# Optimization experiments

Hardware: AMD Instinct MI355X
Metric: run time of the kernel (lower is better)

## Reference

```python
import jax, jax.numpy as jnp
import numpy as np

V, E_DIM, H, B, T = 390, 256, 512, 64, 512
START = 388


def setup_inputs() -> dict:
    key = jax.random.key(0)
    ks = jax.random.split(key, 32)
    s = 0.05
    rn = lambda k, shape: jax.random.normal(k, shape, jnp.float32) * s
    inp = {
        "input": jax.random.normal(ks[0], (B, T, V), jnp.float32),
        # encoder params
        "enc_emb": rn(ks[1], (V, E_DIM)),
        "enc_Wih0": rn(ks[2], (3 * H, E_DIM)),
        "enc_Whh0": rn(ks[3], (3 * H, H)),
        "enc_bih0": rn(ks[4], (3 * H,)),
        "enc_bhh0": rn(ks[5], (3 * H,)),
        "enc_Wih1": rn(ks[6], (3 * H, H)),
        "enc_Whh1": rn(ks[7], (3 * H, H)),
        "enc_bih1": rn(ks[8], (3 * H,)),
        "enc_bhh1": rn(ks[9], (3 * H,)),
        # decoder params
        "dec_emb": rn(ks[10], (V, E_DIM)),
        "dec_Wih0": rn(ks[11], (3 * H, E_DIM)),
        "dec_Whh0": rn(ks[12], (3 * H, H)),
        "dec_bih0": rn(ks[13], (3 * H,)),
        "dec_bhh0": rn(ks[14], (3 * H,)),
        "dec_Wih1": rn(ks[15], (3 * H, H)),
        "dec_Whh1": rn(ks[16], (3 * H, H)),
        "dec_bih1": rn(ks[17], (3 * H,)),
        "dec_bhh1": rn(ks[18], (3 * H,)),
        # prediction head
        "Wp1": rn(ks[19], (H, H)),
        "bp1": rn(ks[20], (H,)),
        "Wp2": rn(ks[21], (V, H)),
        "bp2": rn(ks[22], (V,)),
    }
    return inp


def _gru_cell(x, h, Wih, Whh, bih, bhh):
    # PyTorch GRU cell: gates ordered (r, z, n)
    gi = x @ Wih.T + bih
    gh = h @ Whh.T + bhh
    ir, iz, inn = jnp.split(gi, 3, axis=-1)
    hr, hz, hn = jnp.split(gh, 3, axis=-1)
    r = jax.nn.sigmoid(ir + hr)
    z = jax.nn.sigmoid(iz + hz)
    n = jnp.tanh(inn + r * hn)
    return (1.0 - z) * n + z * h


def reference(input, enc_emb, enc_Wih0, enc_Whh0, enc_bih0, enc_bhh0,
              enc_Wih1, enc_Whh1, enc_bih1, enc_bhh1,
              dec_emb, dec_Wih0, dec_Whh0, dec_bih0, dec_bhh0,
              dec_Wih1, dec_Whh1, dec_bih1, dec_bhh1,
              Wp1, bp1, Wp2, bp2):
    batch, max_len, vocab = input.shape
    hdim = enc_Whh0.shape[1]

    # ---- Encoder: soft embedding + 2-layer GRU, keep final hidden states ----
    x = jnp.einsum('btv,ve->bte', input, enc_emb)  # [B,T,E]
    xt = jnp.transpose(x, (1, 0, 2))               # time-major [T,B,E]
    h0 = jnp.zeros((batch, hdim), input.dtype)

    def step0(h, xt_):
        h = _gru_cell(xt_, h, enc_Wih0, enc_Whh0, enc_bih0, enc_bhh0)
        return h, h
    h1_enc, seq1 = jax.lax.scan(step0, h0, xt)

    def step1(h, xt_):
        h = _gru_cell(xt_, h, enc_Wih1, enc_Whh1, enc_bih1, enc_bhh1)
        return h, None
    h2_enc, _ = jax.lax.scan(step1, h0, seq1)

    tok0 = jnp.full((batch,), START, jnp.int32)
    rng0 = jax.random.key(42)

    def dec_step(carry, _):
        h1, h2, tok, rng = carry
        rng, sk = jax.random.split(rng)
        xe = dec_emb[tok]                               # [B,E]
        h1 = _gru_cell(xe, h1, dec_Wih0, dec_Whh0, dec_bih0, dec_bhh0)
        h2 = _gru_cell(h1, h2, dec_Wih1, dec_Whh1, dec_bih1, dec_bhh1)
        hid = h2 @ Wp1.T + bp1
        hid = jnp.where(hid >= 0, hid, 0.1 * hid)       # LeakyReLU(0.1)
        logits = hid @ Wp2.T + bp2                      # temp=1 -> logits/temp == logits
        probs = jax.nn.softmax(logits, axis=-1)
        tok = jax.random.categorical(sk, logits, axis=-1).astype(jnp.int32)
        return (h1, h2, tok, rng), (probs, tok)

    _, (probs_seq, toks) = jax.lax.scan(
        dec_step, (h1_enc, h2_enc, tok0, rng0), None, length=max_len - 1)

    start_oh = jax.nn.one_hot(tok0, vocab, dtype=input.dtype)  # [B,V]
    outputs = jnp.concatenate(
        [start_oh[:, None, :], jnp.transpose(probs_seq, (1, 0, 2))], axis=1)
    max_output = jnp.concatenate(
        [jnp.full((batch, 1), float(START), jnp.float32),
         toks.T.astype(jnp.float32)], axis=1)
    return outputs, max_output
```

## Files before the change

kernel.cpp:

```cpp
#include <hip/hip_runtime.h>
#include <math.h>


#define BB 64
#define TT 512
#define VV 390
#define EE 256
#define HH 512

#define SW(k, b) ((((k) >> 2) << 8) + ((b) << 2) + ((k) & 3))

static __device__ __forceinline__ void tf2x32(unsigned k0, unsigned k1,
                                              unsigned x0, unsigned x1,
                                              unsigned &o0, unsigned &o1) {
  unsigned ks2 = k0 ^ k1 ^ 0x1BD11BDAu;
  x0 += k0; x1 += k1;
#define TFR(r) x0 += x1; x1 = (x1 << (r)) | (x1 >> (32 - (r))); x1 ^= x0;
  TFR(13) TFR(15) TFR(26) TFR(6)
  x0 += k1; x1 += ks2 + 1u;
  TFR(17) TFR(29) TFR(16) TFR(24)
  x0 += ks2; x1 += k0 + 2u;
  TFR(13) TFR(15) TFR(26) TFR(6)
  x0 += k0; x1 += k1 + 3u;
  TFR(17) TFR(29) TFR(16) TFR(24)
  x0 += k1; x1 += ks2 + 4u;
  TFR(13) TFR(15) TFR(26) TFR(6)
  x0 += ks2; x1 += k0 + 5u;
#undef TFR
  o0 = x0; o1 = x1;
}

static __device__ __forceinline__ float sigm(float x) {
  return 1.0f / (1.0f + expf(-x));
}

static __device__ __forceinline__ unsigned ldu_a(const unsigned* p) {
  return __hip_atomic_load((unsigned*)p, __ATOMIC_RELAXED,
                           __HIP_MEMORY_SCOPE_AGENT);
}
static __device__ __forceinline__ void stu_a(unsigned* p, unsigned v) {
  __hip_atomic_store(p, v, __ATOMIC_RELAXED, __HIP_MEMORY_SCOPE_AGENT);
}
static __device__ __forceinline__ float ldf_a(const float* p) {
  return __uint_as_float(ldu_a((const unsigned*)p));
}
static __device__ __forceinline__ void stf_a(float* p, float v) {
  stu_a((unsigned*)p, __float_as_uint(v));
}
static __device__ __forceinline__ float2 ldf2_a(const float* p) {
  unsigned long long v = __hip_atomic_load((unsigned long long*)p,
      __ATOMIC_RELAXED, __HIP_MEMORY_SCOPE_AGENT);
  return make_float2(__uint_as_float((unsigned)v),
                     __uint_as_float((unsigned)(v >> 32)));
}

static __device__ __forceinline__ void stage512(const float* X, int b0,
                                                float2* L) {
  int tid = threadIdx.x;
  float2 v[8];
#pragma unroll
  for (int r = 0; r < 8; ++r) {
    int i = tid + (r << 8);
    v[r] = ldf2_a(X + ((i >> 4) << 8) + ((b0 + ((i >> 1) & 7)) << 2) +
                  ((i & 1) << 1));
  }
#pragma unroll
  for (int r = 0; r < 8; ++r) L[tid + (r << 8)] = v[r];
}

template <int K>
static __device__ __forceinline__ void dot3_lds(const float4* Lx, int bi,
    const float* __restrict__ w0, const float* __restrict__ w1,
    const float* __restrict__ w2, float &r0, float &r1, float &r2) {
  const float4* q0 = (const float4*)w0;
  const float4* q1 = (const float4*)w1;
  const float4* q2 = (const float4*)w2;
  float s0 = 0.f, s1 = 0.f, s2 = 0.f;
#pragma unroll
  for (int k4 = 0; k4 < (K >> 2); ++k4) {
    float4 x = Lx[(k4 << 3) + bi];
    float4 u0 = q0[k4], u1 = q1[k4], u2 = q2[k4];
    s0 = fmaf(x.x, u0.x, s0); s0 = fmaf(x.y, u0.y, s0); s0 = fmaf(x.z, u0.z, s0); s0 = fmaf(x.w, u0.w, s0);
    s1 = fmaf(x.x, u1.x, s1); s1 = fmaf(x.y, u1.y, s1); s1 = fmaf(x.z, u1.z, s1); s1 = fmaf(x.w, u1.w, s1);
    s2 = fmaf(x.x, u2.x, s2); s2 = fmaf(x.y, u2.y, s2); s2 = fmaf(x.z, u2.z, s2); s2 = fmaf(x.w, u2.w, s2);
  }
  r0 = s0; r1 = s1; r2 = s2;
}

template <int K>
static __device__ __forceinline__ float dot1_lds(const float4* Lx, int bi,
    const float* __restrict__ w) {
  const float4* q = (const float4*)w;
  float s = 0.f;
#pragma unroll
  for (int k4 = 0; k4 < (K >> 2); ++k4) {
    float4 x = Lx[(k4 << 3) + bi];
    float4 u = q[k4];
    s = fmaf(x.x, u.x, s); s = fmaf(x.y, u.y, s);
    s = fmaf(x.z, u.z, s); s = fmaf(x.w, u.w, s);
  }
  return s;
}

template <int K>
static __device__ __forceinline__ void dot3s_p(const float* __restrict__ X, int b,
    const float* __restrict__ w0, const float* __restrict__ w1,
    const float* __restrict__ w2, float &r0, float &r1, float &r2) {
  const float4* q0 = (const float4*)w0;
  const float4* q1 = (const float4*)w1;
  const float4* q2 = (const float4*)w2;
  const float4* Xp = (const float4*)X;
  float s0 = 0.f, s1 = 0.f, s2 = 0.f;
#pragma unroll
  for (int k4 = 0; k4 < (K >> 2); ++k4) {
    float4 x = Xp[(k4 << 6) + b];
    float4 u0 = q0[k4], u1 = q1[k4], u2 = q2[k4];
    s0 = fmaf(x.x, u0.x, s0); s0 = fmaf(x.y, u0.y, s0); s0 = fmaf(x.z, u0.z, s0); s0 = fmaf(x.w, u0.w, s0);
    s1 = fmaf(x.x, u1.x, s1); s1 = fmaf(x.y, u1.y, s1); s1 = fmaf(x.z, u1.z, s1); s1 = fmaf(x.w, u1.w, s1);
    s2 = fmaf(x.x, u2.x, s2); s2 = fmaf(x.y, u2.y, s2); s2 = fmaf(x.z, u2.z, s2); s2 = fmaf(x.w, u2.w, s2);
  }
  r0 = s0; r1 = s1; r2 = s2;
}

template <int K>
static __device__ __forceinline__ void dot3_row(const float* __restrict__ xrow,
    const float* __restrict__ w0, const float* __restrict__ w1,
    const float* __restrict__ w2, float &r0, float &r1, float &r2) {
  const float4* xq = (const float4*)xrow;
  const float4* q0 = (const float4*)w0;
  const float4* q1 = (const float4*)w1;
  const float4* q2 = (const float4*)w2;
  float s0 = 0.f, s1 = 0.f, s2 = 0.f;
#pragma unroll
  for (int k4 = 0; k4 < (K >> 2); ++k4) {
    float4 x = xq[k4];
    float4 u0 = q0[k4], u1 = q1[k4], u2 = q2[k4];
    s0 = fmaf(x.x, u0.x, s0); s0 = fmaf(x.y, u0.y, s0); s0 = fmaf(x.z, u0.z, s0); s0 = fmaf(x.w, u0.w, s0);
    s1 = fmaf(x.x, u1.x, s1); s1 = fmaf(x.y, u1.y, s1); s1 = fmaf(x.z, u1.z, s1); s1 = fmaf(x.w, u1.w, s1);
    s2 = fmaf(x.x, u2.x, s2); s2 = fmaf(x.y, u2.y, s2); s2 = fmaf(x.z, u2.z, s2); s2 = fmaf(x.w, u2.w, s2);
  }
  r0 = s0; r1 = s1; r2 = s2;
}

static __device__ __forceinline__ void gbar(unsigned* f, int nwg, int wgi,
                                            unsigned ep) {
  __syncthreads();
  int tid = threadIdx.x;
  if (tid == 0) stu_a(f + wgi, ep);
  if (tid < 64) {
    bool ok;
    do {
      ok = true;
      for (int i = tid; i < nwg; i += 64) ok &= (ldu_a(f + i) >= ep);
    } while (!__all((int)ok));
  }
  __syncthreads();
}

__global__ __launch_bounds__(256) void k_init(float* out,
    float* h1buf, float* h2buf, int* tok, unsigned* ebase) {
  int wg = blockIdx.x, tid = threadIdx.x;
  for (int i = wg * 256 + tid; i < HH * BB; i += 64 * 256) {
    h1buf[i] = 0.f;
    h2buf[i] = 0.f;
  }
  for (int v = tid; v < VV; v += 256)
    out[(size_t)wg * TT * VV + v] = (v == 388) ? 1.0f : 0.0f;
  if (wg == 0) {
    ebase[tid] = 0u;
    ebase[tid + 256] = 0u;
  }
  if (tid == 0) {
    out[(size_t)BB * TT * VV + (size_t)wg * TT] = 388.0f;
    tok[wg] = 388;
  }
}

__global__ __launch_bounds__(256) void k_xgemm(const float* __restrict__ input,
    const float* __restrict__ emb, float* __restrict__ xT) {
  int t = blockIdx.x, tid = threadIdx.x;
  int s = tid >> 6, b = tid & 63;
  __shared__ float lin[64 * 65];
  float4 acc[16];
#pragma unroll
  for (int i = 0; i < 16; ++i) acc[i] = make_float4(0.f, 0.f, 0.f, 0.f);
  for (int k0 = 0; k0 < VV; k0 += 64) {
    int kmax = min(64, VV - k0);
    __syncthreads();
#pragma unroll
    for (int r = 0; r < 16; ++r) {
      int idx = r * 256 + tid;
      int b2 = idx >> 6, kk = idx & 63;
      if (kk < kmax)
        lin[kk * 65 + b2] = input[((size_t)b2 * TT + t) * VV + k0 + kk];
    }
    __syncthreads();
    for (int kk = 0; kk < kmax; ++kk) {
      float xv = lin[kk * 65 + b];
      const float4* er = (const float4*)(emb + (size_t)(k0 + kk) * EE);
#pragma unroll
      for (int i = 0; i < 16; ++i) {
        float4 w = er[s + 4 * i];
        acc[i].x = fmaf(xv, w.x, acc[i].x);
        acc[i].y = fmaf(xv, w.y, acc[i].y);
        acc[i].z = fmaf(xv, w.z, acc[i].z);
        acc[i].w = fmaf(xv, w.w, acc[i].w);
      }
    }
  }
  float* dst0 = xT + (size_t)t * (EE * 64);
#pragma unroll
  for (int i = 0; i < 16; ++i)
    *(float4*)(dst0 + (s + 4 * i) * 256 + 4 * b) = acc[i];
}

__global__ __launch_bounds__(256, 2) void k_enc(
    const float* xT, float* h1buf, float* h2buf,
    const float* __restrict__ Wih0, const float* __restrict__ Whh0,
    const float* __restrict__ bih0, const float* __restrict__ bhh0,
    const float* __restrict__ Wih1, const float* __restrict__ Whh1,
    const float* __restrict__ bih1, const float* __restrict__ bhh1,
    unsigned* eflags, unsigned* dflags) {
  int wg = blockIdx.x, tid = threadIdx.x;
  int g = wg >> 6, wgi = wg & 63;
  int b0 = g << 3;
  int lay = wgi >> 5, j0 = (wgi & 31) << 4;
  int task = tid >> 7, l = tid & 127;
  int jj = l >> 3, bi = l & 7;
  int j = j0 + jj, b = b0 + bi;
  __shared__ float2 sX[2048];
  __shared__ float2 sY[2048];
  __shared__ float part[3][128];
  unsigned* gf = eflags + (g << 6);
  for (int t = 0; t <= TT; ++t) {
    const float* h1_r = h1buf + (t & 1) * (HH * BB);
    float* h1_w = h1buf + ((t + 1) & 1) * (HH * BB);
    if (lay == 0) {
      if (t < TT) {
        stage512(h1_r, b0, sX);
        __syncthreads();
        float ar = 0.f, az = 0.f, an = 0.f;
        if (task == 0) {
          dot3s_p<EE>(xT + (size_t)t * (EE * 64), b,
                      Wih0 + (size_t)j * EE, Wih0 + (size_t)(512 + j) * EE,
                      Wih0 + (size_t)(1024 + j) * EE, ar, az, an);
        } else {
          float hr, hz, hn;
          dot3_lds<HH>((const float4*)sX, bi,
                       Whh0 + (size_t)j * HH, Whh0 + (size_t)(512 + j) * HH,
                       Whh0 + (size_t)(1024 + j) * HH, hr, hz, hn);
          part[0][l] = hr; part[1][l] = hz; part[2][l] = hn;
        }
        __syncthreads();
        if (task == 0) {
          float hr = part[0][l], hz = part[1][l], hn = part[2][l];
          float r = sigm((ar + bih0[j]) + (hr + bhh0[j]));
          float z = sigm((az + bih0[512 + j]) + (hz + bhh0[512 + j]));
          float n = tanhf((an + bih0[1024 + j]) + r * (hn + bhh0[1024 + j]));
          float hp = ((const float*)sX)[((j >> 2) << 5) + (bi << 2) + (j & 3)];
          stf_a(h1_w + SW(j, b), (1.0f - z) * n + z * hp);
        }
      }
    } else {
      if (t >= 1) {
        const float* h2_r = h2buf + ((t + 1) & 1) * (HH * BB);
        float* h2_w = h2buf + (t & 1) * (HH * BB);
        stage512(h1_r, b0, sX);
        stage512(h2_r, b0, sY);
        __syncthreads();
        float ar = 0.f, az = 0.f, an = 0.f;
        if (task == 0) {
          dot3_lds<HH>((const float4*)sX, bi,
                       Wih1 + (size_t)j * HH, Wih1 + (size_t)(512 + j) * HH,
                       Wih1 + (size_t)(1024 + j) * HH, ar, az, an);
        } else {
          float hr, hz, hn;
          dot3_lds<HH>((const float4*)sY, bi,
                       Whh1 + (size_t)j * HH, Whh1 + (size_t)(512 + j) * HH,
                       Whh1 + (size_t)(1024 + j) * HH, hr, hz, hn);
          part[0][l] = hr; part[1][l] = hz; part[2][l] = hn;
        }
        __syncthreads();
        if (task == 0) {
          float hr = part[0][l], hz = part[1][l], hn = part[2][l];
          float r = sigm((ar + bih1[j]) + (hr + bhh1[j]));
          float z = sigm((az + bih1[512 + j]) + (hz + bhh1[512 + j]));
          float n = tanhf((an + bih1[1024 + j]) + r * (hn + bhh1[1024 + j]));
          float hp = ((const float*)sY)[((j >> 2) << 5) + (bi << 2) + (j & 3)];
          stf_a(h2_w + SW(j, b), (1.0f - z) * n + z * hp);
        }
      }
    }
    if (t == 2 && wgi == 0 && tid < 32) stu_a(dflags + (g << 5) + tid, 0u);
    if (t < TT) gbar(gf, 64, wgi, (unsigned)(t + 1));
  }
}

__global__ __launch_bounds__(256, 1) void k_dec(
    float* h1buf, float* h2buf,
    const float* __restrict__ demb,
    const float* __restrict__ dWih0, const float* __restrict__ dWhh0,
    const float* __restrict__ dbih0, const float* __restrict__ dbhh0,
    const float* __restrict__ dWih1, const float* __restrict__ dWhh1,
    const float* __restrict__ dbih1, const float* __restrict__ dbhh1,
    const float* __restrict__ Wp1, const float* __restrict__ bp1,
    const float* __restrict__ Wp2, const float* __restrict__ bp2,
    float* out, int* tok, unsigned* dflags, float* hid) {
  int wg = blockIdx.x, tid = threadIdx.x;
  int g = wg >> 5, wgi = wg & 31;
  int b0 = g << 3, j0 = wgi << 4;
  int task = tid >> 7, l = tid & 127;
  int jj = l >> 3, bi = l & 7;
  int j = j0 + jj, b = b0 + bi;
  __shared__ float2 sX[2048];
  __shared__ float2 sY[2048];
  __shared__ float part[3][128];
  __shared__ __align__(16) float lhid[HH];
  __shared__ float rf[8];
  __shared__ int ri[4];
  unsigned* gf = dflags + (g << 5);
  unsigned rk0 = 0u, rk1 = 42u;
  unsigned ep = 0u;
  for (int d = 0; d < TT - 1; ++d) {
    const float* h1_r = h1buf + (d & 1) * (HH * BB);
    float* h1_w = h1buf + ((d + 1) & 1) * (HH * BB);
    const float* h2_r = h2buf + (d & 1) * (HH * BB);
    float* h2_w = h2buf + ((d + 1) & 1) * (HH * BB);
    {
      stage512(h1_r, b0, sX);
      __syncthreads();
      float ar = 0.f, az = 0.f, an = 0.f;
      if (task == 1) {
        float hr, hz, hn;
        dot3_lds<HH>((const float4*)sX, bi,
                     dWhh0 + (size_t)j * HH, dWhh0 + (size_t)(512 + j) * HH,
                     dWhh0 + (size_t)(1024 + j) * HH, hr, hz, hn);
        part[0][l] = hr; part[1][l] = hz; part[2][l] = hn;
      } else {
        int tk = (int)ldu_a((const unsigned*)tok + b);
        dot3_row<EE>(demb + (size_t)tk * EE,
                     dWih0 + (size_t)j * EE, dWih0 + (size_t)(512 + j) * EE,
                     dWih0 + (size_t)(1024 + j) * EE, ar, az, an);
      }
      __syncthreads();
      if (task == 0) {
        float hr = part[0][l], hz = part[1][l], hn = part[2][l];
        float r = sigm((ar + dbih0[j]) + (hr + dbhh0[j]));
        float z = sigm((az + dbih0[512 + j]) + (hz + dbhh0[512 + j]));
        float n = tanhf((an + dbih0[1024 + j]) + r * (hn + dbhh0[1024 + j]));
        float hp = ((const float*)sX)[((j >> 2) << 5) + (bi << 2) + (j & 3)];
        stf_a(h1_w + SW(j, b), (1.0f - z) * n + z * hp);
      }
    }
    gbar(gf, 32, wgi, ++ep);
    {
      stage512(h1_w, b0, sX);
      stage512(h2_r, b0, sY);
      __syncthreads();
      float ar = 0.f, az = 0.f, an = 0.f;
      if (task == 0) {
        dot3_lds<HH>((const float4*)sX, bi,
                     dWih1 + (size_t)j * HH, dWih1 + (size_t)(512 + j) * HH,
                     dWih1 + (size_t)(1024 + j) * HH, ar, az, an);
      } else {
        float hr, hz, hn;
        dot3_lds<HH>((const float4*)sY, bi,
                     dWhh1 + (size_t)j * HH, dWhh1 + (size_t)(512 + j) * HH,
                     dWhh1 + (size_t)(1024 + j) * HH, hr, hz, hn);
        part[0][l] = hr; part[1][l] = hz; part[2][l] = hn;
      }
      __syncthreads();
      if (task == 0) {
        float hr = part[0][l], hz = part[1][l], hn = part[2][l];
        float r = sigm((ar + dbih1[j]) + (hr + dbhh1[j]));
        float z = sigm((az + dbih1[512 + j]) + (hz + dbhh1[512 + j]));
        float n = tanhf((an + dbih1[1024 + j]) + r * (hn + dbhh1[1024 + j]));
        float hp = ((const float*)sY)[((j >> 2) << 5) + (bi << 2) + (j & 3)];
        stf_a(h2_w + SW(j, b), (1.0f - z) * n + z * hp);
      }
    }
    gbar(gf, 32, wgi, ++ep);
    {
      stage512(h2_w, b0, sX);
      __syncthreads();
      if (tid < 128) {
        float a = dot1_lds<HH>((const float4*)sX, bi, Wp1 + (size_t)j * HH);
        a += bp1[j];
        stf_a(hid + SW(j, b), (a >= 0.f) ? a : 0.1f * a);
      }
    }
    gbar(gf, 32, wgi, ++ep);
    if (wgi < 8) {
      int brow = b0 + wgi;
      if (tid < 128) {
        float2 ha = ldf2_a(hid + tid * 256 + brow * 4);
        float2 hb = ldf2_a(hid + tid * 256 + brow * 4 + 2);
        lhid[4 * tid] = ha.x; lhid[4 * tid + 1] = ha.y;
        lhid[4 * tid + 2] = hb.x; lhid[4 * tid + 3] = hb.y;
      }
      __syncthreads();
      float v0 = 0.f, v1 = 0.f;
      if (tid < VV) {
        const float4* w = (const float4*)(Wp2 + (size_t)tid * HH);
        float a = 0.f;
#pragma unroll 8
        for (int k4 = 0; k4 < HH / 4; ++k4) {
          float4 q = w[k4];
          float4 hv = *(const float4*)&lhid[k4 * 4];
          a = fmaf(hv.x, q.x, a); a = fmaf(hv.y, q.y, a);
          a = fmaf(hv.z, q.z, a); a = fmaf(hv.w, q.w, a);
        }
        v0 = a + bp2[tid];
      }
      if (tid + 256 < VV) {
        const float4* w = (const float4*)(Wp2 + (size_t)(tid + 256) * HH);
        float a = 0.f;
#pragma unroll 8
        for (int k4 = 0; k4 < HH / 4; ++k4) {
          float4 q = w[k4];
          float4 hv = *(const float4*)&lhid[k4 * 4];
          a = fmaf(hv.x, q.x, a); a = fmaf(hv.y, q.y, a);
          a = fmaf(hv.z, q.z, a); a = fmaf(hv.w, q.w, a);
        }
        v1 = a + bp2[tid + 256];
      }
      float m = -INFINITY;
      if (tid < VV) m = fmaxf(m, v0);
      if (tid + 256 < VV) m = fmaxf(m, v1);
      for (int off = 32; off > 0; off >>= 1) m = fmaxf(m, __shfl_down(m, off, 64));
      if ((tid & 63) == 0) rf[tid >> 6] = m;
      __syncthreads();
      if (tid == 0) rf[4] = fmaxf(fmaxf(rf[0], rf[1]), fmaxf(rf[2], rf[3]));
      __syncthreads();
      m = rf[4];
      unsigned sk0, sk1;
      tf2x32(rk0, rk1, 0u, 1u, sk0, sk1);
      float by = -INFINITY; int bc = 0x7fffffff;
      if (tid < VV) {
        unsigned o0, o1;
        tf2x32(sk0, sk1, 0u, (unsigned)(brow * VV + tid), o0, o1);
        unsigned bits = o0 ^ o1;
        float f = __uint_as_float(0x3f800000u | (bits >> 9)) - 1.0f;
        float u = (f > 0.f) ? f : 1.17549435e-38f;
        float gg = (float)(-log(-log((double)u)));
        float y = v0 + gg;
        if (y > by || (y == by && tid < bc)) { by = y; bc = tid; }
      }
      if (tid + 256 < VV) {
        int c = tid + 256;
        unsigned o0, o1;
        tf2x32(sk0, sk1, 0u, (unsigned)(brow * VV + c), o0, o1);
        unsigned bits = o0 ^ o1;
        float f = __uint_as_float(0x3f800000u | (bits >> 9)) - 1.0f;
        float u = (f > 0.f) ? f : 1.17549435e-38f;
        float gg = (float)(-log(-log((double)u)));
        float y = v1 + gg;
        if (y > by || (y == by && c < bc)) { by = y; bc = c; }
      }
      for (int off = 32; off > 0; off >>= 1) {
        float oy = __shfl_down(by, off, 64);
        int oc = __shfl_down(bc, off, 64);
        if (oy > by || (oy == by && oc < bc)) { by = oy; bc = oc; }
      }
      if ((tid & 63) == 0) { rf[tid >> 6] = by; ri[tid >> 6] = bc; }
      __syncthreads();
      if (tid == 0) {
        by = rf[0]; bc = ri[0];
        for (int w2 = 1; w2 < 4; ++w2)
          if (rf[w2] > by || (rf[w2] == by && ri[w2] < bc)) { by = rf[w2]; bc = ri[w2]; }
        stu_a((unsigned*)tok + brow, (unsigned)bc);
        out[(size_t)BB * TT * VV + (size_t)brow * TT + (d + 1)] = (float)bc;
      }
      __syncthreads();
      float e0 = 0.f, e1 = 0.f, ssum = 0.f;
      if (tid < VV) { e0 = expf(v0 - m); ssum += e0; }
      if (tid + 256 < VV) { e1 = expf(v1 - m); ssum += e1; }
      for (int off = 32; off > 0; off >>= 1) ssum += __shfl_down(ssum, off, 64);
      if ((tid & 63) == 0) rf[tid >> 6] = ssum;
      __syncthreads();
      if (tid == 0) rf[4] = (rf[0] + rf[1]) + (rf[2] + rf[3]);
      __syncthreads();
      float S = rf[4];
      float* orow = out + ((size_t)brow * TT + (d + 1)) * VV;
      if (tid < VV) orow[tid] = e0 / S;
      if (tid + 256 < VV) orow[tid + 256] = e1 / S;
    }
    {
      unsigned n0, n1;
      tf2x32(rk0, rk1, 0u, 0u, n0, n1);
      rk0 = n0; rk1 = n1;
    }
    if (d < TT - 2) gbar(gf, 32, wgi, ++ep);
  }
}

extern "C" void kernel_launch(void* const* d_in, const int* in_sizes, int n_in,
                              void* d_out, int out_size, void* d_ws, size_t ws_size,
                              hipStream_t stream) {
  (void)in_sizes; (void)n_in; (void)out_size; (void)ws_size;
  const float* input = (const float*)d_in[0];
  const float* e_emb = (const float*)d_in[1];
  const float* eWih0 = (const float*)d_in[2];
  const float* eWhh0 = (const float*)d_in[3];
  const float* ebih0 = (const float*)d_in[4];
  const float* ebhh0 = (const float*)d_in[5];
  const float* eWih1 = (const float*)d_in[6];
  const float* eWhh1 = (const float*)d_in[7];
  const float* ebih1 = (const float*)d_in[8];
  const float* ebhh1 = (const float*)d_in[9];
  const float* d_emb = (const float*)d_in[10];
  const float* dWih0 = (const float*)d_in[11];
  const float* dWhh0 = (const float*)d_in[12];
  const float* dbih0 = (const float*)d_in[13];
  const float* dbhh0 = (const float*)d_in[14];
  const float* dWih1 = (const float*)d_in[15];
  const float* dWhh1 = (const float*)d_in[16];
  const float* dbih1 = (const float*)d_in[17];
  const float* dbhh1 = (const float*)d_in[18];
  const float* Wp1   = (const float*)d_in[19];
  const float* bp1   = (const float*)d_in[20];
  const float* Wp2   = (const float*)d_in[21];
  const float* bp2   = (const float*)d_in[22];
  float* out = (float*)d_out;

  float* xT = (float*)d_ws;
  float* h1buf = xT + (size_t)TT * EE * 64;
  float* h2buf = h1buf + 2 * HH * BB;
  int* tok = (int*)(h2buf + 2 * HH * BB);
  unsigned* eflags = (unsigned*)(out + ((size_t)1 * TT + 1) * VV);
  unsigned* dflags = (unsigned*)xT;
  float* hid = xT + 4096;

  k_init<<<64, 256, 0, stream>>>(out, h1buf, h2buf, tok, eflags);
  k_xgemm<<<TT, 256, 0, stream>>>(input, e_emb, xT);
  k_enc<<<512, 256, 0, stream>>>(xT, h1buf, h2buf,
      eWih0, eWhh0, ebih0, ebhh0, eWih1, eWhh1, ebih1, ebhh1, eflags, dflags);
  k_dec<<<256, 256, 0, stream>>>(h1buf, h2buf, d_emb,
      dWih0, dWhh0, dbih0, dbhh0, dWih1, dWhh1, dbih1, dbhh1,
      Wp1, bp1, Wp2, bp2, out, tok, dflags, hid);
}
```

Before: 73.42 ms.

## Restructure decoder step to precompute recurrent matvecs and drop a grid barrier

The decoder loop now computes the Whh0/Whh1 recurrent matvecs for the next step at the end of the current step, so each step's critical path carries only the input-side GEMV. The Wp1 projection is computed redundantly inside the head workgroups, which removes the global hid buffer and one grid barrier per step. Staging loads are rotated per workgroup to spread memory contention, and the barrier spin adds s_sleep. In exchange the head workgroups take on extra Wp1 work, and both task halves now run full 512-wide dot products.

```diff
diff --git a/kernel.cpp b/kernel.cpp
--- a/kernel.cpp
+++ b/kernel.cpp
@@ -41,9 +41,6 @@
 static __device__ __forceinline__ void stu_a(unsigned* p, unsigned v) {
   __hip_atomic_store(p, v, __ATOMIC_RELAXED, __HIP_MEMORY_SCOPE_AGENT);
 }
-static __device__ __forceinline__ float ldf_a(const float* p) {
-  return __uint_as_float(ldu_a((const unsigned*)p));
-}
 static __device__ __forceinline__ void stf_a(float* p, float v) {
   stu_a((unsigned*)p, __float_as_uint(v));
 }
@@ -55,17 +52,20 @@
 }
 
 static __device__ __forceinline__ void stage512(const float* X, int b0,
-                                                float2* L) {
+                                                float2* L, int rot) {
   int tid = threadIdx.x;
   float2 v[8];
 #pragma unroll
   for (int r = 0; r < 8; ++r) {
-    int i = tid + (r << 8);
-    v[r] = ldf2_a(X + ((i >> 4) << 8) + ((b0 + ((i >> 1) & 7)) << 2) +
-                  ((i & 1) << 1));
-  }
-#pragma unroll
-  for (int r = 0; r < 8; ++r) L[tid + (r << 8)] = v[r];
+    int idx = tid + (((r + rot) & 7) << 8);
+    v[r] = ldf2_a(X + ((idx >> 4) << 8) + ((b0 + ((idx >> 1) & 7)) << 2) +
+                  ((idx & 1) << 1));
+  }
+#pragma unroll
+  for (int r = 0; r < 8; ++r) {
+    int idx = tid + (((r + rot) & 7) << 8);
+    L[idx] = v[r];
+  }
 }
 
 template <int K>
@@ -148,11 +148,13 @@
   int tid = threadIdx.x;
   if (tid == 0) stu_a(f + wgi, ep);
   if (tid < 64) {
-    bool ok;
-    do {
-      ok = true;
+    bool done = false;
+    while (!done) {
+      bool ok = true;
       for (int i = tid; i < nwg; i += 64) ok &= (ldu_a(f + i) >= ep);
-    } while (!__all((int)ok));
+      done = __all((int)ok);
+      if (!done) __builtin_amdgcn_s_sleep(1);
+    }
   }
   __syncthreads();
 }
@@ -228,6 +230,7 @@
   int task = tid >> 7, l = tid & 127;
   int jj = l >> 3, bi = l & 7;
   int j = j0 + jj, b = b0 + bi;
+  int rot = wg & 7;
   __shared__ float2 sX[2048];
   __shared__ float2 sY[2048];
   __shared__ float part[3][128];
@@ -237,7 +240,7 @@
     float* h1_w = h1buf + ((t + 1) & 1) * (HH * BB);
     if (lay == 0) {
       if (t < TT) {
-        stage512(h1_r, b0, sX);
+        stage512(h1_r, b0, sX, rot);
         __syncthreads();
         float ar = 0.f, az = 0.f, an = 0.f;
         if (task == 0) {
@@ -265,8 +268,8 @@
       if (t >= 1) {
         const float* h2_r = h2buf + ((t + 1) & 1) * (HH * BB);
         float* h2_w = h2buf + (t & 1) * (HH * BB);
-        stage512(h1_r, b0, sX);
-        stage512(h2_r, b0, sY);
+        stage512(h1_r, b0, sX, rot);
+        stage512(h2_r, b0, sY, rot);
         __syncthreads();
         float ar = 0.f, az = 0.f, an = 0.f;
         if (task == 0) {
@@ -305,98 +308,88 @@
     const float* __restrict__ dbih1, const float* __restrict__ dbhh1,
     const float* __restrict__ Wp1, const float* __restrict__ bp1,
     const float* __restrict__ Wp2, const float* __restrict__ bp2,
-    float* out, int* tok, unsigned* dflags, float* hid) {
+    float* out, int* tok, unsigned* dflags) {
   int wg = blockIdx.x, tid = threadIdx.x;
   int g = wg >> 5, wgi = wg & 31;
   int b0 = g << 3, j0 = wgi << 4;
   int task = tid >> 7, l = tid & 127;
   int jj = l >> 3, bi = l & 7;
   int j = j0 + jj, b = b0 + bi;
+  int rot = wgi & 7;
   __shared__ float2 sX[2048];
   __shared__ float2 sY[2048];
-  __shared__ float part[3][128];
+  __shared__ float pA[3][128];
+  __shared__ float pB[3][128];
   __shared__ __align__(16) float lhid[HH];
   __shared__ float rf[8];
   __shared__ int ri[4];
+  __shared__ int ltok[8];
   unsigned* gf = dflags + (g << 5);
   unsigned rk0 = 0u, rk1 = 42u;
   unsigned ep = 0u;
+  stage512(h1buf, b0, sX, rot);
+  stage512(h2buf, b0, sY, rot);
+  __syncthreads();
+  if (task == 1) {
+    float hr, hz, hn;
+    dot3_lds<HH>((const float4*)sX, bi,
+                 dWhh0 + (size_t)j * HH, dWhh0 + (size_t)(512 + j) * HH,
+                 dWhh0 + (size_t)(1024 + j) * HH, hr, hz, hn);
+    pA[0][l] = hr; pA[1][l] = hz; pA[2][l] = hn;
+  } else {
+    float hr, hz, hn;
+    dot3_lds<HH>((const float4*)sY, bi,
+                 dWhh1 + (size_t)j * HH, dWhh1 + (size_t)(512 + j) * HH,
+                 dWhh1 + (size_t)(1024 + j) * HH, hr, hz, hn);
+    pB[0][l] = hr; pB[1][l] = hz; pB[2][l] = hn;
+  }
+  __syncthreads();
   for (int d = 0; d < TT - 1; ++d) {
-    const float* h1_r = h1buf + (d & 1) * (HH * BB);
     float* h1_w = h1buf + ((d + 1) & 1) * (HH * BB);
-    const float* h2_r = h2buf + (d & 1) * (HH * BB);
     float* h2_w = h2buf + ((d + 1) & 1) * (HH * BB);
-    {
-      stage512(h1_r, b0, sX);
-      __syncthreads();
-      float ar = 0.f, az = 0.f, an = 0.f;
-      if (task == 1) {
-        float hr, hz, hn;
-        dot3_lds<HH>((const float4*)sX, bi,
-                     dWhh0 + (size_t)j * HH, dWhh0 + (size_t)(512 + j) * HH,
-                     dWhh0 + (size_t)(1024 + j) * HH, hr, hz, hn);
-        part[0][l] = hr; part[1][l] = hz; part[2][l] = hn;
-      } else {
-        int tk = (int)ldu_a((const unsigned*)tok + b);
-        dot3_row<EE>(demb + (size_t)tk * EE,
-                     dWih0 + (size_t)j * EE, dWih0 + (size_t)(512 + j) * EE,
-                     dWih0 + (size_t)(1024 + j) * EE, ar, az, an);
-      }
-      __syncthreads();
-      if (task == 0) {
-        float hr = part[0][l], hz = part[1][l], hn = part[2][l];
-        float r = sigm((ar + dbih0[j]) + (hr + dbhh0[j]));
-        float z = sigm((az + dbih0[512 + j]) + (hz + dbhh0[512 + j]));
-        float n = tanhf((an + dbih0[1024 + j]) + r * (hn + dbhh0[1024 + j]));
-        float hp = ((const float*)sX)[((j >> 2) << 5) + (bi << 2) + (j & 3)];
-        stf_a(h1_w + SW(j, b), (1.0f - z) * n + z * hp);
-      }
+    if (tid < 8) ltok[tid] = (int)ldu_a((const unsigned*)tok + b0 + tid);
+    __syncthreads();
+    if (task == 0) {
+      int tk = ltok[bi];
+      float ar, az, an;
+      dot3_row<EE>(demb + (size_t)tk * EE,
+                   dWih0 + (size_t)j * EE, dWih0 + (size_t)(512 + j) * EE,
+                   dWih0 + (size_t)(1024 + j) * EE, ar, az, an);
+      float hr = pA[0][l], hz = pA[1][l], hn = pA[2][l];
+      float r = sigm((ar + dbih0[j]) + (hr + dbhh0[j]));
+      float z = sigm((az + dbih0[512 + j]) + (hz + dbhh0[512 + j]));
+      float n = tanhf((an + dbih0[1024 + j]) + r * (hn + dbhh0[1024 + j]));
+      float hp = ((const float*)sX)[((j >> 2) << 5) + (bi << 2) + (j & 3)];
+      stf_a(h1_w + SW(j, b), (1.0f - z) * n + z * hp);
     }
     gbar(gf, 32, wgi, ++ep);
-    {
-      stage512(h1_w, b0, sX);
-      stage512(h2_r, b0, sY);
-      __syncthreads();
-      float ar = 0.f, az = 0.f, an = 0.f;
-      if (task == 0) {
-        dot3_lds<HH>((const float4*)sX, bi,
-                     dWih1 + (size_t)j * HH, dWih1 + (size_t)(512 + j) * HH,
-                     dWih1 + (size_t)(1024 + j) * HH, ar, az, an);
-      } else {
-        float hr, hz, hn;
-        dot3_lds<HH>((const float4*)sY, bi,
-                     dWhh1 + (size_t)j * HH, dWhh1 + (size_t)(512 + j) * HH,
-                     dWhh1 + (size_t)(1024 + j) * HH, hr, hz, hn);
-        part[0][l] = hr; part[1][l] = hz; part[2][l] = hn;
-      }
-      __syncthreads();
-      if (task == 0) {
-        float hr = part[0][l], hz = part[1][l], hn = part[2][l];
-        float r = sigm((ar + dbih1[j]) + (hr + dbhh1[j]));
-        float z = sigm((az + dbih1[512 + j]) + (hz + dbhh1[512 + j]));
-        float n = tanhf((an + dbih1[1024 + j]) + r * (hn + dbhh1[1024 + j]));
-        float hp = ((const float*)sY)[((j >> 2) << 5) + (bi << 2) + (j & 3)];
-        stf_a(h2_w + SW(j, b), (1.0f - z) * n + z * hp);
-      }
+    stage512(h1_w, b0, sX, rot);
+    __syncthreads();
+    if (task == 0) {
+      float ar, az, an;
+      dot3_lds<HH>((const float4*)sX, bi,
+                   dWih1 + (size_t)j * HH, dWih1 + (size_t)(512 + j) * HH,
+                   dWih1 + (size_t)(1024 + j) * HH, ar, az, an);
+      float hr = pB[0][l], hz = pB[1][l], hn = pB[2][l];
+      float r = sigm((ar + dbih1[j]) + (hr + dbhh1[j]));
+      float z = sigm((az + dbih1[512 + j]) + (hz + dbhh1[512 + j]));
+      float n = tanhf((an + dbih1[1024 + j]) + r * (hn + dbhh1[1024 + j]));
+      float hp = ((const float*)sY)[((j >> 2) << 5) + (bi << 2) + (j & 3)];
+      stf_a(h2_w + SW(j, b), (1.0f - z) * n + z * hp);
     }
     gbar(gf, 32, wgi, ++ep);
-    {
-      stage512(h2_w, b0, sX);
-      __syncthreads();
-      if (tid < 128) {
-        float a = dot1_lds<HH>((const float4*)sX, bi, Wp1 + (size_t)j * HH);
-        a += bp1[j];
-        stf_a(hid + SW(j, b), (a >= 0.f) ? a : 0.1f * a);
-      }
-    }
-    gbar(gf, 32, wgi, ++ep);
+    stage512(h2_w, b0, sY, rot);
+    __syncthreads();
     if (wgi < 8) {
       int brow = b0 + wgi;
-      if (tid < 128) {
-        float2 ha = ldf2_a(hid + tid * 256 + brow * 4);
-        float2 hb = ldf2_a(hid + tid * 256 + brow * 4 + 2);
-        lhid[4 * tid] = ha.x; lhid[4 * tid + 1] = ha.y;
-        lhid[4 * tid + 2] = hb.x; lhid[4 * tid + 3] = hb.y;
+      {
+        float a = dot1_lds<HH>((const float4*)sY, wgi, Wp1 + (size_t)tid * HH);
+        a += bp1[tid];
+        lhid[tid] = (a >= 0.f) ? a : 0.1f * a;
+        float a2 = dot1_lds<HH>((const float4*)sY, wgi,
+                                Wp1 + (size_t)(tid + 256) * HH);
+        a2 += bp1[tid + 256];
+        lhid[tid + 256] = (a2 >= 0.f) ? a2 : 0.1f * a2;
       }
       __syncthreads();
       float v0 = 0.f, v1 = 0.f;
@@ -484,13 +477,27 @@
       float* orow = out + ((size_t)brow * TT + (d + 1)) * VV;
       if (tid < VV) orow[tid] = e0 / S;
       if (tid + 256 < VV) orow[tid + 256] = e1 / S;
+      __syncthreads();
+    }
+    if (task == 1) {
+      float hr, hz, hn;
+      dot3_lds<HH>((const float4*)sX, bi,
+                   dWhh0 + (size_t)j * HH, dWhh0 + (size_t)(512 + j) * HH,
+                   dWhh0 + (size_t)(1024 + j) * HH, hr, hz, hn);
+      pA[0][l] = hr; pA[1][l] = hz; pA[2][l] = hn;
+    } else {
+      float hr, hz, hn;
+      dot3_lds<HH>((const float4*)sY, bi,
+                   dWhh1 + (size_t)j * HH, dWhh1 + (size_t)(512 + j) * HH,
+                   dWhh1 + (size_t)(1024 + j) * HH, hr, hz, hn);
+      pB[0][l] = hr; pB[1][l] = hz; pB[2][l] = hn;
     }
     {
       unsigned n0, n1;
       tf2x32(rk0, rk1, 0u, 0u, n0, n1);
       rk0 = n0; rk1 = n1;
     }
-    if (d < TT - 2) gbar(gf, 32, wgi, ++ep);
+    gbar(gf, 32, wgi, ++ep);
   }
 }
 
@@ -529,7 +536,6 @@
   int* tok = (int*)(h2buf + 2 * HH * BB);
   unsigned* eflags = (unsigned*)(out + ((size_t)1 * TT + 1) * VV);
   unsigned* dflags = (unsigned*)xT;
-  float* hid = xT + 4096;
 
   k_init<<<64, 256, 0, stream>>>(out, h1buf, h2buf, tok, eflags);
   k_xgemm<<<TT, 256, 0, stream>>>(input, e_emb, xT);
@@ -537,5 +543,5 @@
       eWih0, eWhh0, ebih0, ebhh0, eWih1, eWhh1, ebih1, ebhh1, eflags, dflags);
   k_dec<<<256, 256, 0, stream>>>(h1buf, h2buf, d_emb,
       dWih0, dWhh0, dbih0, dbhh0, dWih1, dWhh1, dbih1, dbhh1,
-      Wp1, bp1, Wp2, bp2, out, tok, dflags, hid);
-}
+      Wp1, bp1, Wp2, bp2, out, tok, dflags);
+}
```

Measured after the change: 119.0 ms. 1.62x slower.
